# Performance work log

Hardware: AMD Instinct MI355X
Metric: run time of the kernel (lower is better)

## Reference

```python
import jax, jax.numpy as jnp
import numpy as np

HID = 512
BATCH = 64
SRC_LEN = 2048


def setup_inputs() -> dict:
    key = jax.random.key(0)
    ks = jax.random.split(key, 8)
    s = 1.0 / np.sqrt(HID)
    return {
        "h": jax.random.normal(ks[0], (1, BATCH, HID), dtype=jnp.float32),
        "enc_out": jax.random.normal(ks[1], (BATCH, SRC_LEN, HID), dtype=jnp.float32),
        "W1_w": jax.random.uniform(ks[2], (HID, HID), jnp.float32, -s, s),
        "W1_b": jax.random.uniform(ks[3], (HID,), jnp.float32, -s, s),
        "W2_w": jax.random.uniform(ks[4], (HID, HID), jnp.float32, -s, s),
        "W2_b": jax.random.uniform(ks[5], (HID,), jnp.float32, -s, s),
        "V_w": jax.random.uniform(ks[6], (1, HID), jnp.float32, -s, s),
        "V_b": jax.random.uniform(ks[7], (1,), jnp.float32, -s, s),
    }


def reference(h, enc_out, W1_w, W1_b, W2_w, W2_b, V_w, V_b):
    # h: [1, B, H] -> [B, 1, H]; broadcast against enc_out: [B, S, H]
    h_b = jnp.transpose(h, (1, 0, 2))                       # [B, 1, H]
    proj_enc = jnp.einsum('bsh,oh->bso', enc_out, W1_w) + W1_b  # [B, S, H]
    proj_h = jnp.einsum('bqh,oh->bqo', h_b, W2_w) + W2_b        # [B, 1, H]
    energy = jnp.tanh(proj_enc + proj_h)                        # [B, S, H]
    scores = jnp.einsum('bsh,oh->bso', energy, V_w)[..., 0] + V_b[0]  # [B, S]
    return jax.nn.softmax(scores, axis=1)
```

## Files before the change

kernel.cpp:

```cpp
#include <hip/hip_runtime.h>
#include <hip/hip_bf16.h>

#define HID   512
#define BATCH 64
#define SRC   2048
#define MROWS (BATCH * SRC)

typedef __bf16 bf16x8 __attribute__((ext_vector_type(8)));
typedef __bf16 bf16x4 __attribute__((ext_vector_type(4)));
typedef float  f32x16 __attribute__((ext_vector_type(16)));

#define PANEL 520

__device__ inline float fast_tanh(float x) {
    float e = __builtin_amdgcn_exp2f(x * 2.8853900817779268f);
    return 1.0f - 2.0f * __builtin_amdgcn_rcpf(e + 1.0f);
}

__global__ void pack_w1(const float* __restrict__ W1w, __bf16* __restrict__ Bpk) {
    int t = blockIdx.x * 256 + threadIdx.x;
    int l = t & 63, tile = t >> 6;
    int ot = tile & 15, kt = tile >> 4;
    int o = ot * 32 + (l & 31);
    int k = kt * 16 + (l >> 5) * 8;
    const float* src = W1w + (size_t)o * HID + k;
    float4 v0 = *(const float4*)src;
    float4 v1 = *(const float4*)(src + 4);
    bf16x8 r;
    r[0]=(__bf16)v0.x; r[1]=(__bf16)v0.y; r[2]=(__bf16)v0.z; r[3]=(__bf16)v0.w;
    r[4]=(__bf16)v1.x; r[5]=(__bf16)v1.y; r[6]=(__bf16)v1.z; r[7]=(__bf16)v1.w;
    ((bf16x8*)Bpk)[t] = r;
}

__global__ void prep_bias(const float* __restrict__ h, const float* __restrict__ W2w,
                          const float* __restrict__ W2b, const float* __restrict__ W1b,
                          float* __restrict__ biasc) {
    int b = blockIdx.x;
    int tid = threadIdx.x;
    __shared__ float hh[HID];
    hh[tid]       = h[b * HID + tid];
    hh[tid + 256] = h[b * HID + tid + 256];
    __syncthreads();
    const float4* h4 = (const float4*)hh;
    for (int o = tid; o < HID; o += 256) {
        const float4* w4 = (const float4*)(W2w + (size_t)o * HID);
        float s = 0.f;
        #pragma unroll 8
        for (int k = 0; k < HID / 4; ++k) {
            float4 a = h4[k]; float4 w = w4[k];
            s += a.x * w.x + a.y * w.y + a.z * w.z + a.w * w.w;
        }
        biasc[b * HID + o] = s + W2b[o] + W1b[o];
    }
}

__global__ __launch_bounds__(512, 4) void attn_main(
        const float* __restrict__ enc, const __bf16* __restrict__ Bpk,
        const float* __restrict__ biasc, const float* __restrict__ Vw,
        float* __restrict__ scores) {
    __shared__ __bf16 AL[64 * PANEL];
    __shared__ float sred[64][9];

    const int tid = threadIdx.x;
    const int blockRow = blockIdx.x * 64;
    const int b = blockIdx.x >> 5;
    const int lane = tid & 63;
    const int wv = tid >> 6;
    const int col = lane & 31;
    const int hfi = lane >> 5;

    const int o0 = (2 * wv) * 32 + col;
    const int o1 = o0 + 32;
    float bb0 = biasc[b * HID + o0], bb1 = biasc[b * HID + o1];
    float vv0 = Vw[o0],               vv1 = Vw[o1];

    const float4* encB = (const float4*)enc + (size_t)blockRow * 128;
    #pragma unroll
    for (int i = 0; i < 16; ++i) {
        int f = i * 512 + tid;
        float4 v = encB[f];
        int row = f >> 7;
        int kq  = (f & 127) << 2;
        int kt = kq >> 4, half = (kq >> 3) & 1, j = kq & 7;
        int off = (kt * 2 + (row >> 5)) * PANEL + ((row & 31) + 32 * half) * 8 + j;
        bf16x4 o4;
        o4[0]=(__bf16)v.x; o4[1]=(__bf16)v.y; o4[2]=(__bf16)v.z; o4[3]=(__bf16)v.w;
        *(bf16x4*)&AL[off] = o4;
    }
    __syncthreads();

    const bf16x8* pB0 = (const bf16x8*)Bpk + (size_t)(2 * wv) * 64 + lane;
    const bf16x8* pB1 = pB0 + 64;
    const __bf16* pA  = AL + lane * 8;

    f32x16 acc00, acc01, acc10, acc11;
    #pragma unroll
    for (int i = 0; i < 16; ++i) { acc00[i]=0.f; acc01[i]=0.f; acc10[i]=0.f; acc11[i]=0.f; }

    bf16x8 b0 = pB0[0];
    bf16x8 b1 = pB1[0];
    #pragma unroll 4
    for (int kt = 0; kt < 32; ++kt) {
        int nk = (kt < 31) ? (kt + 1) : 31;
        bf16x8 nb0 = pB0[(size_t)nk * 1024];
        bf16x8 nb1 = pB1[(size_t)nk * 1024];
        bf16x8 a0 = *(const bf16x8*)(pA + kt * (2 * PANEL));
        bf16x8 a1 = *(const bf16x8*)(pA + kt * (2 * PANEL) + PANEL);
        acc00 = __builtin_amdgcn_mfma_f32_32x32x16_bf16(a0, b0, acc00, 0, 0, 0);
        acc10 = __builtin_amdgcn_mfma_f32_32x32x16_bf16(a1, b0, acc10, 0, 0, 0);
        acc01 = __builtin_amdgcn_mfma_f32_32x32x16_bf16(a0, b1, acc01, 0, 0, 0);
        acc11 = __builtin_amdgcn_mfma_f32_32x32x16_bf16(a1, b1, acc11, 0, 0, 0);
        b0 = nb0; b1 = nb1;
    }

    float p0[16], p1[16];
    #pragma unroll
    for (int r = 0; r < 16; ++r) {
        p0[r] = vv0 * fast_tanh(acc00[r] + bb0) + vv1 * fast_tanh(acc01[r] + bb1);
        p1[r] = vv0 * fast_tanh(acc10[r] + bb0) + vv1 * fast_tanh(acc11[r] + bb1);
    }
    #pragma unroll
    for (int m = 1; m <= 16; m <<= 1) {
        #pragma unroll
        for (int r = 0; r < 16; ++r) {
            p0[r] += __shfl_xor(p0[r], m, 64);
            p1[r] += __shfl_xor(p1[r], m, 64);
        }
    }
    if (col == 0) {
        #pragma unroll
        for (int r = 0; r < 16; ++r) {
            int rl = (r & 3) + 8 * (r >> 2) + 4 * hfi;
            sred[rl][wv]      = p0[r];
            sred[32 + rl][wv] = p1[r];
        }
    }
    __syncthreads();
    if (tid < 64) {
        float s = 0.f;
        #pragma unroll
        for (int w = 0; w < 8; ++w) s += sred[tid][w];
        scores[blockRow + tid] = s;
    }
}

__global__ void softmax_k(float* __restrict__ scores) {
    int b = blockIdx.x;
    int tid = threadIdx.x;
    int lane = tid & 63, wv = tid >> 6;
    __shared__ float red[4];
    float* row = scores + (size_t)b * SRC;
    float4 v0 = *(float4*)(row + tid * 8);
    float4 v1 = *(float4*)(row + tid * 8 + 4);
    float x[8] = {v0.x, v0.y, v0.z, v0.w, v1.x, v1.y, v1.z, v1.w};
    float mx = x[0];
    #pragma unroll
    for (int r = 1; r < 8; ++r) mx = fmaxf(mx, x[r]);
    #pragma unroll
    for (int m = 1; m <= 32; m <<= 1) mx = fmaxf(mx, __shfl_xor(mx, m, 64));
    if (lane == 0) red[wv] = mx;
    __syncthreads();
    mx = fmaxf(fmaxf(red[0], red[1]), fmaxf(red[2], red[3]));
    __syncthreads();
    float s = 0.f;
    #pragma unroll
    for (int r = 0; r < 8; ++r) {
        x[r] = __builtin_amdgcn_exp2f((x[r] - mx) * 1.44269504088896f);
        s += x[r];
    }
    #pragma unroll
    for (int m = 1; m <= 32; m <<= 1) s += __shfl_xor(s, m, 64);
    if (lane == 0) red[wv] = s;
    __syncthreads();
    s = red[0] + red[1] + red[2] + red[3];
    float inv = 1.0f / s;
    float4 o0 = make_float4(x[0] * inv, x[1] * inv, x[2] * inv, x[3] * inv);
    float4 o1 = make_float4(x[4] * inv, x[5] * inv, x[6] * inv, x[7] * inv);
    *(float4*)(row + tid * 8)     = o0;
    *(float4*)(row + tid * 8 + 4) = o1;
}

extern "C" void kernel_launch(void* const* d_in, const int* in_sizes, int n_in,
                              void* d_out, int out_size, void* d_ws, size_t ws_size,
                              hipStream_t stream) {
    const float* h    = (const float*)d_in[0];
    const float* enc  = (const float*)d_in[1];
    const float* W1w  = (const float*)d_in[2];
    const float* W1b  = (const float*)d_in[3];
    const float* W2w  = (const float*)d_in[4];
    const float* W2b  = (const float*)d_in[5];
    const float* Vw   = (const float*)d_in[6];
    float* out = (float*)d_out;

    __bf16* Bpk  = (__bf16*)d_ws;
    float*  biasc = (float*)((char*)d_ws + HID * HID * sizeof(__bf16));

    pack_w1  <<<128, 256, 0, stream>>>(W1w, Bpk);
    prep_bias<<<BATCH, 256, 0, stream>>>(h, W2w, W2b, W1b, biasc);
    attn_main<<<MROWS / 64, 512, 0, stream>>>(enc, Bpk, biasc, Vw, out);
    softmax_k<<<BATCH, 256, 0, stream>>>(out);
}
```

Baseline: 491.5 us.

## Merge prep kernels, rotate K start per block, use DPP reductions

```diff
diff --git a/kernel.cpp b/kernel.cpp
--- a/kernel.cpp
+++ b/kernel.cpp
@@ -17,40 +17,56 @@
     return 1.0f - 2.0f * __builtin_amdgcn_rcpf(e + 1.0f);
 }
 
-__global__ void pack_w1(const float* __restrict__ W1w, __bf16* __restrict__ Bpk) {
-    int t = blockIdx.x * 256 + threadIdx.x;
-    int l = t & 63, tile = t >> 6;
-    int ot = tile & 15, kt = tile >> 4;
-    int o = ot * 32 + (l & 31);
-    int k = kt * 16 + (l >> 5) * 8;
-    const float* src = W1w + (size_t)o * HID + k;
-    float4 v0 = *(const float4*)src;
-    float4 v1 = *(const float4*)(src + 4);
-    bf16x8 r;
-    r[0]=(__bf16)v0.x; r[1]=(__bf16)v0.y; r[2]=(__bf16)v0.z; r[3]=(__bf16)v0.w;
-    r[4]=(__bf16)v1.x; r[5]=(__bf16)v1.y; r[6]=(__bf16)v1.z; r[7]=(__bf16)v1.w;
-    ((bf16x8*)Bpk)[t] = r;
-}
-
-__global__ void prep_bias(const float* __restrict__ h, const float* __restrict__ W2w,
-                          const float* __restrict__ W2b, const float* __restrict__ W1b,
-                          float* __restrict__ biasc) {
-    int b = blockIdx.x;
+template <int CTRL>
+__device__ inline float dpp_add(float x) {
+    int y = __builtin_amdgcn_update_dpp(0, __builtin_bit_cast(int, x), CTRL, 0xF, 0xF, true);
+    return x + __builtin_bit_cast(float, y);
+}
+
+__device__ inline float reduce32(float x) {
+    x = dpp_add<0xB1>(x);
+    x = dpp_add<0x4E>(x);
+    x = dpp_add<0x141>(x);
+    x = dpp_add<0x140>(x);
+    int y = __builtin_amdgcn_ds_swizzle(__builtin_bit_cast(int, x), 0x401F);
+    return x + __builtin_bit_cast(float, y);
+}
+
+__global__ void prep(const float* __restrict__ W1w, __bf16* __restrict__ Bpk,
+                     const float* __restrict__ h, const float* __restrict__ W2w,
+                     const float* __restrict__ W2b, const float* __restrict__ W1b,
+                     float* __restrict__ biasc) {
+    __shared__ float hh[HID];
     int tid = threadIdx.x;
-    __shared__ float hh[HID];
-    hh[tid]       = h[b * HID + tid];
-    hh[tid + 256] = h[b * HID + tid + 256];
-    __syncthreads();
-    const float4* h4 = (const float4*)hh;
-    for (int o = tid; o < HID; o += 256) {
-        const float4* w4 = (const float4*)(W2w + (size_t)o * HID);
-        float s = 0.f;
-        #pragma unroll 8
-        for (int k = 0; k < HID / 4; ++k) {
-            float4 a = h4[k]; float4 w = w4[k];
-            s += a.x * w.x + a.y * w.y + a.z * w.z + a.w * w.w;
+    if (blockIdx.x < 128) {
+        int t = blockIdx.x * 256 + tid;
+        int l = t & 63, tile = t >> 6;
+        int ot = tile & 15, kt = tile >> 4;
+        int o = ot * 32 + (l & 31);
+        int k = kt * 16 + (l >> 5) * 8;
+        const float* src = W1w + (size_t)o * HID + k;
+        float4 v0 = *(const float4*)src;
+        float4 v1 = *(const float4*)(src + 4);
+        bf16x8 r;
+        r[0]=(__bf16)v0.x; r[1]=(__bf16)v0.y; r[2]=(__bf16)v0.z; r[3]=(__bf16)v0.w;
+        r[4]=(__bf16)v1.x; r[5]=(__bf16)v1.y; r[6]=(__bf16)v1.z; r[7]=(__bf16)v1.w;
+        ((bf16x8*)Bpk)[t] = r;
+    } else {
+        int b = blockIdx.x - 128;
+        hh[tid]       = h[b * HID + tid];
+        hh[tid + 256] = h[b * HID + tid + 256];
+        __syncthreads();
+        const float4* h4 = (const float4*)hh;
+        for (int o = tid; o < HID; o += 256) {
+            const float4* w4 = (const float4*)(W2w + (size_t)o * HID);
+            float s = 0.f;
+            #pragma unroll 8
+            for (int k = 0; k < HID / 4; ++k) {
+                float4 a = h4[k]; float4 w = w4[k];
+                s += a.x * w.x + a.y * w.y + a.z * w.z + a.w * w.w;
+            }
+            biasc[b * HID + o] = s + W2b[o] + W1b[o];
         }
-        biasc[b * HID + o] = s + W2b[o] + W1b[o];
     }
 }
 
@@ -89,23 +105,25 @@
     }
     __syncthreads();
 
-    const bf16x8* pB0 = (const bf16x8*)Bpk + (size_t)(2 * wv) * 64 + lane;
-    const bf16x8* pB1 = pB0 + 64;
-    const __bf16* pA  = AL + lane * 8;
+    const int rot = blockIdx.x & 31;
+    const char* BpkB = (const char*)Bpk + (2 * wv) * 1024 + lane * 16;
+    const __bf16* pA = AL + lane * 8;
 
     f32x16 acc00, acc01, acc10, acc11;
     #pragma unroll
     for (int i = 0; i < 16; ++i) { acc00[i]=0.f; acc01[i]=0.f; acc10[i]=0.f; acc11[i]=0.f; }
 
-    bf16x8 b0 = pB0[0];
-    bf16x8 b1 = pB1[0];
-    #pragma unroll 4
+    bf16x8 b0 = *(const bf16x8*)(BpkB + (size_t)rot * 16384);
+    bf16x8 b1 = *(const bf16x8*)(BpkB + (size_t)rot * 16384 + 1024);
+    #pragma unroll 8
     for (int kt = 0; kt < 32; ++kt) {
-        int nk = (kt < 31) ? (kt + 1) : 31;
-        bf16x8 nb0 = pB0[(size_t)nk * 1024];
-        bf16x8 nb1 = pB1[(size_t)nk * 1024];
-        bf16x8 a0 = *(const bf16x8*)(pA + kt * (2 * PANEL));
-        bf16x8 a1 = *(const bf16x8*)(pA + kt * (2 * PANEL) + PANEL);
+        int in = (kt + 1 + rot) & 31;
+        bf16x8 nb0 = *(const bf16x8*)(BpkB + (size_t)in * 16384);
+        bf16x8 nb1 = *(const bf16x8*)(BpkB + (size_t)in * 16384 + 1024);
+        int ia = (kt + rot) & 31;
+        const __bf16* pa = pA + ia * (2 * PANEL);
+        bf16x8 a0 = *(const bf16x8*)pa;
+        bf16x8 a1 = *(const bf16x8*)(pa + PANEL);
         acc00 = __builtin_amdgcn_mfma_f32_32x32x16_bf16(a0, b0, acc00, 0, 0, 0);
         acc10 = __builtin_amdgcn_mfma_f32_32x32x16_bf16(a1, b0, acc10, 0, 0, 0);
         acc01 = __builtin_amdgcn_mfma_f32_32x32x16_bf16(a0, b1, acc01, 0, 0, 0);
@@ -113,26 +131,16 @@
         b0 = nb0; b1 = nb1;
     }
 
-    float p0[16], p1[16];
     #pragma unroll
     for (int r = 0; r < 16; ++r) {
-        p0[r] = vv0 * fast_tanh(acc00[r] + bb0) + vv1 * fast_tanh(acc01[r] + bb1);
-        p1[r] = vv0 * fast_tanh(acc10[r] + bb0) + vv1 * fast_tanh(acc11[r] + bb1);
-    }
-    #pragma unroll
-    for (int m = 1; m <= 16; m <<= 1) {
-        #pragma unroll
-        for (int r = 0; r < 16; ++r) {
-            p0[r] += __shfl_xor(p0[r], m, 64);
-            p1[r] += __shfl_xor(p1[r], m, 64);
-        }
-    }
-    if (col == 0) {
-        #pragma unroll
-        for (int r = 0; r < 16; ++r) {
+        float p0 = vv0 * fast_tanh(acc00[r] + bb0) + vv1 * fast_tanh(acc01[r] + bb1);
+        float p1 = vv0 * fast_tanh(acc10[r] + bb0) + vv1 * fast_tanh(acc11[r] + bb1);
+        p0 = reduce32(p0);
+        p1 = reduce32(p1);
+        if (col == 0) {
             int rl = (r & 3) + 8 * (r >> 2) + 4 * hfi;
-            sred[rl][wv]      = p0[r];
-            sred[32 + rl][wv] = p1[r];
+            sred[rl][wv]      = p0;
+            sred[32 + rl][wv] = p1;
         }
     }
     __syncthreads();
@@ -195,8 +203,7 @@
     __bf16* Bpk  = (__bf16*)d_ws;
     float*  biasc = (float*)((char*)d_ws + HID * HID * sizeof(__bf16));
 
-    pack_w1  <<<128, 256, 0, stream>>>(W1w, Bpk);
-    prep_bias<<<BATCH, 256, 0, stream>>>(h, W2w, W2b, W1b, biasc);
+    prep     <<<192, 256, 0, stream>>>(W1w, Bpk, h, W2w, W2b, W1b, biasc);
     attn_main<<<MROWS / 64, 512, 0, stream>>>(enc, Bpk, biasc, Vw, out);
     softmax_k<<<BATCH, 256, 0, stream>>>(out);
 }
```

New measurement: 443.8 us. -9.7%, faster.
